# Optimization experiments

Hardware: AMD Instinct MI355X
Metric: run time of the kernel (lower is better)

The kernel has to match this reference:

```python
import jax, jax.numpy as jnp
import numpy as np

N, L, D = 2, 2048, 1024
H, KV, HD = 16, 4, 64
CAP = 50.0


def _rope_cache(L, hd):
    inv_freq = 1.0 / (10000.0 ** (np.arange(0, hd, 2, dtype=np.float32) / hd))
    t = np.arange(L, dtype=np.float32)
    freqs = np.outer(t, inv_freq)                      # (L, hd/2)
    emb = np.concatenate([freqs, freqs], axis=-1)      # (L, hd)
    return jnp.asarray(np.cos(emb)), jnp.asarray(np.sin(emb))


def setup_inputs() -> dict:
    key = jax.random.key(0)
    ks = jax.random.split(key, 6)
    s = 0.02
    cos, sin = _rope_cache(L, HD)
    return {
        "x": jax.random.normal(ks[0], (N, L, D), jnp.float32),
        "Wq": jax.random.normal(ks[1], (D, H * HD), jnp.float32) * s,
        "bq": jnp.zeros((H * HD,), jnp.float32),
        "Wk": jax.random.normal(ks[2], (D, KV * HD), jnp.float32) * s,
        "bk": jnp.zeros((KV * HD,), jnp.float32),
        "Wv": jax.random.normal(ks[3], (D, KV * HD), jnp.float32) * s,
        "bv": jnp.zeros((KV * HD,), jnp.float32),
        "Wo": jax.random.normal(ks[4], (D, D), jnp.float32) * s,
        "bo": jnp.zeros((D,), jnp.float32),
        "q_gamma": jnp.ones((H, HD), jnp.float32),
        "k_gamma": jnp.ones((KV, HD), jnp.float32),
        "rope_cos": cos,
        "rope_sin": sin,
        "is_causal": 1,
    }


def _rmsnorm(t, gamma):
    # t: (N, heads, L, HD); gamma: (heads, HD)
    inv = jax.lax.rsqrt(jnp.mean(t * t, axis=-1, keepdims=True) + 1e-6)
    return t * inv * gamma[None, :, None, :]


def _apply_rope(t, cos, sin):
    # t: (N, heads, L, HD); cos/sin: (L, HD)
    hd = t.shape[-1]
    t1, t2 = t[..., : hd // 2], t[..., hd // 2:]
    rot = jnp.concatenate([-t2, t1], axis=-1)
    return t * cos[None, None] + rot * sin[None, None]


def reference(x, Wq, bq, Wk, bk, Wv, bv, Wo, bo, q_gamma, k_gamma, rope_cos, rope_sin, is_causal):
    n, l, d = x.shape
    h, hd = q_gamma.shape
    kv = k_gamma.shape[0]
    n_rep = h // kv

    q = (x @ Wq + bq).reshape(n, l, h, hd).transpose(0, 2, 1, 3)   # (n,h,l,hd)
    k = (x @ Wk + bk).reshape(n, l, kv, hd).transpose(0, 2, 1, 3)  # (n,kv,l,hd)
    v = (x @ Wv + bv).reshape(n, l, kv, hd).transpose(0, 2, 1, 3)

    q = _rmsnorm(q, q_gamma)
    k = _rmsnorm(k, k_gamma)
    q = _apply_rope(q, rope_cos, rope_sin)
    k = _apply_rope(k, rope_cos, rope_sin)

    if n_rep > 1:
        k = jnp.repeat(k, n_rep, axis=1)
        v = jnp.repeat(v, n_rep, axis=1)

    scale = hd ** -0.5
    logits = jnp.einsum("bhqd,bhkd->bhqk", q, k) * scale
    logits = CAP * jnp.tanh(logits / CAP)
    if is_causal:
        causal = jnp.tril(jnp.ones((l, l), dtype=bool))
        logits = jnp.where(causal[None, None], logits, -jnp.inf)
    weights = jax.nn.softmax(logits, axis=-1)
    y = jnp.einsum("bhqk,bhkd->bhqd", weights, v)
    y = y.transpose(0, 2, 1, 3).reshape(n, l, d)
    return y @ Wo + bo
```

## Files before the change

kernel.cpp:

```cpp
#include <hip/hip_runtime.h>
#include <hip/hip_bf16.h>

typedef __attribute__((ext_vector_type(8))) short short8;
typedef __attribute__((ext_vector_type(4))) float f32x4;

using bf16 = __hip_bfloat16;

#define L_SEQ 2048
#define NB 2
#define DM 1024
#define NH 16
#define NKV 4
#define HDIM 64
#define CAPV 50.0f

#if __has_builtin(__builtin_amdgcn_exp2f)
#define EXP2(x) __builtin_amdgcn_exp2f(x)
#else
#define EXP2(x) exp2f(x)
#endif

__device__ __forceinline__ unsigned short f2bs(float f) {
  bf16 h = __float2bfloat16(f);
  return __builtin_bit_cast(unsigned short, h);
}

__device__ __forceinline__ float bs2f(unsigned short u) {
  return __bfloat162float(__builtin_bit_cast(bf16, u));
}

__device__ __forceinline__ void gload_lds16(const void* g, void* l) {
  __builtin_amdgcn_global_load_lds(
      (const __attribute__((address_space(1))) void*)g,
      (__attribute__((address_space(3))) void*)l, 16, 0, 0);
}

__global__ void k_cvt_x(const float* __restrict__ x, ushort* __restrict__ xb) {
  int i = (blockIdx.x * blockDim.x + threadIdx.x) * 4;
  float4 v = *reinterpret_cast<const float4*>(x + i);
  ushort4 o = make_ushort4(f2bs(v.x), f2bs(v.y), f2bs(v.z), f2bs(v.w));
  *reinterpret_cast<ushort4*>(xb + i) = o;
}

__global__ void k_transpose_all(const float* __restrict__ Wq, const float* __restrict__ Wk,
                                const float* __restrict__ Wv, const float* __restrict__ Wo,
                                bf16* __restrict__ wqt, bf16* __restrict__ wkt,
                                bf16* __restrict__ wvt, bf16* __restrict__ wot) {
  __shared__ float tile[32][33];
  const int z = blockIdx.z;
  const float* W = (z == 0) ? Wq : (z == 1) ? Wk : (z == 2) ? Wv : Wo;
  bf16* Wt = (z == 0) ? wqt : (z == 1) ? wkt : (z == 2) ? wvt : wot;
  const int Ncols = (z == 1 || z == 2) ? 256 : 1024;
  const int bx = blockIdx.x * 32;
  if (bx >= Ncols) return;
  const int by = blockIdx.y * 32;
  const int tx = threadIdx.x, ty = threadIdx.y;
  #pragma unroll
  for (int j = 0; j < 32; j += 8)
    tile[ty + j][tx] = W[(size_t)(by + ty + j) * Ncols + bx + tx];
  __syncthreads();
  #pragma unroll
  for (int j = 0; j < 32; j += 8)
    Wt[(size_t)(bx + ty + j) * 1024 + by + tx] = __float2bfloat16(tile[tx][ty + j]);
}

template<int OUT_MODE>
__global__ __launch_bounds__(256) void k_gemm(const bf16* __restrict__ A,
                                              const bf16* __restrict__ Bt,
                                              const float* __restrict__ bq,
                                              const float* __restrict__ bk,
                                              const float* __restrict__ bv,
                                              const float* __restrict__ qg,
                                              const float* __restrict__ kg,
                                              const float* __restrict__ rcT,
                                              const float* __restrict__ rsT,
                                              void* __restrict__ out0,
                                              void* __restrict__ out1,
                                              void* __restrict__ out2,
                                              int M, int Ncols, int K) {
  __shared__ __align__(16) bf16 As[2][64 * 64];
  __shared__ __align__(16) bf16 Bs[2][128 * 64];
  const int t = threadIdx.x;
  const int lane = t & 63;
  const int w = t >> 6;
  const int wr = w >> 1, wc = w & 1;
  const int m0 = blockIdx.y * 64, n0 = blockIdx.x * 128;
  const int lr = lane & 15, lg = lane >> 4;
  const int nkt = K >> 6;

  f32x4 acc[2][4];
  #pragma unroll
  for (int m = 0; m < 2; ++m)
    #pragma unroll
    for (int n = 0; n < 4; ++n)
      acc[m][n] = f32x4{0.f, 0.f, 0.f, 0.f};

  {
    #pragma unroll
    for (int p = 0; p < 2; ++p) {
      const int Gb = p * 256 + w * 64;
      const int G = Gb + lane;
      const int row = G >> 3, gc = G & 7;
      gload_lds16(&A[(size_t)(m0 + row) * K + ((gc ^ (row & 7)) * 8)], &As[0][Gb * 8]);
    }
    #pragma unroll
    for (int p = 0; p < 4; ++p) {
      const int Gb = p * 256 + w * 64;
      const int G = Gb + lane;
      const int row = G >> 3, gc = G & 7;
      gload_lds16(&Bt[(size_t)(n0 + row) * K + ((gc ^ (row & 7)) * 8)], &Bs[0][Gb * 8]);
    }
  }
  int cur = 0;

  for (int kt = 0; kt < nkt; ++kt) {
    __syncthreads();

    if (kt + 1 < nkt) {
      const int kofs = (kt + 1) * 64;
      #pragma unroll
      for (int p = 0; p < 2; ++p) {
        const int Gb = p * 256 + w * 64;
        const int G = Gb + lane;
        const int row = G >> 3, gc = G & 7;
        gload_lds16(&A[(size_t)(m0 + row) * K + kofs + ((gc ^ (row & 7)) * 8)],
                    &As[cur ^ 1][Gb * 8]);
      }
      #pragma unroll
      for (int p = 0; p < 4; ++p) {
        const int Gb = p * 256 + w * 64;
        const int G = Gb + lane;
        const int row = G >> 3, gc = G & 7;
        gload_lds16(&Bt[(size_t)(n0 + row) * K + kofs + ((gc ^ (row & 7)) * 8)],
                    &Bs[cur ^ 1][Gb * 8]);
      }
    }

    #pragma unroll
    for (int ks = 0; ks < 2; ++ks) {
      short8 af[2], bfr[4];
      #pragma unroll
      for (int m = 0; m < 2; ++m) {
        const int row = wr * 32 + m * 16 + lr;
        af[m] = *reinterpret_cast<const short8*>(
            &As[cur][row * 64 + (((ks * 4 + lg) ^ (row & 7)) * 8)]);
      }
      #pragma unroll
      for (int n = 0; n < 4; ++n) {
        const int row = wc * 64 + n * 16 + lr;
        bfr[n] = *reinterpret_cast<const short8*>(
            &Bs[cur][row * 64 + (((ks * 4 + lg) ^ (row & 7)) * 8)]);
      }
      #pragma unroll
      for (int m = 0; m < 2; ++m)
        #pragma unroll
        for (int n = 0; n < 4; ++n)
          acc[m][n] = __builtin_amdgcn_mfma_f32_16x16x32_bf16(af[m], bfr[n], acc[m][n], 0, 0, 0);
    }
    cur ^= 1;
  }

  const int colbase = n0 + wc * 64;

  if (OUT_MODE == 1) {
    #pragma unroll
    for (int m = 0; m < 2; ++m) {
      const int row = m0 + wr * 32 + m * 16 + lg * 4;
      #pragma unroll
      for (int n = 0; n < 4; ++n) {
        const int col = colbase + n * 16 + lr;
        const float bvv = bq[col];
        #pragma unroll
        for (int r = 0; r < 4; ++r)
          reinterpret_cast<float*>(out0)[(size_t)(row + r) * Ncols + col] = acc[m][n][r] + bvv;
      }
    }
  } else {
    if (colbase >= 1280) {
      #pragma unroll
      for (int m = 0; m < 2; ++m) {
        const int row = m0 + wr * 32 + m * 16 + lg * 4;
        const int bb = row >> 11, l = row & 2047;
        #pragma unroll
        for (int n = 0; n < 4; ++n) {
          const int d = colbase - 1280 + n * 16 + lr;
          const float bvv = bv[d];
          ushort4 o;
          o.x = f2bs(acc[m][n][0] + bvv);
          o.y = f2bs(acc[m][n][1] + bvv);
          o.z = f2bs(acc[m][n][2] + bvv);
          o.w = f2bs(acc[m][n][3] + bvv);
          *reinterpret_cast<ushort4*>(
              &reinterpret_cast<bf16*>(out2)[((size_t)bb * 256 + d) * L_SEQ + l]) = o;
        }
      }
    } else {
      const bool isQ = (colbase < 1024);
      const float* bias = isQ ? bq : bk;
      const float* gma = isQ ? qg : kg;
      bf16* dst0 = reinterpret_cast<bf16*>(isQ ? out0 : out1);
      const int cb = isQ ? colbase : (colbase - 1024);
      const int head = cb >> 6;
      const int heads = isQ ? NH : NKV;
      float g[4];
      #pragma unroll
      for (int n = 0; n < 4; ++n) g[n] = gma[cb + n * 16 + lr];
      #pragma unroll
      for (int m = 0; m < 2; ++m) {
        const int row = m0 + wr * 32 + m * 16 + lg * 4;
        float vv[4][4];
        float ss[4] = {0.f, 0.f, 0.f, 0.f};
        #pragma unroll
        for (int n = 0; n < 4; ++n) {
          const float bvv = bias[cb + n * 16 + lr];
          #pragma unroll
          for (int r = 0; r < 4; ++r) {
            vv[n][r] = acc[m][n][r] + bvv;
            ss[r] = fmaf(vv[n][r], vv[n][r], ss[r]);
          }
        }
        #pragma unroll
        for (int r = 0; r < 4; ++r) {
          float s = ss[r];
          s += __shfl_xor(s, 1, 64);
          s += __shfl_xor(s, 2, 64);
          s += __shfl_xor(s, 4, 64);
          s += __shfl_xor(s, 8, 64);
          ss[r] = rsqrtf(s * (1.0f / 64.0f) + 1e-6f);
        }
        float tv[4][4];
        #pragma unroll
        for (int n = 0; n < 4; ++n)
          #pragma unroll
          for (int r = 0; r < 4; ++r)
            tv[n][r] = vv[n][r] * ss[r] * g[n];
        #pragma unroll
        for (int r = 0; r < 4; ++r) {
          const int grow = row + r;
          const int bb = grow >> 11, l = grow & 2047;
          bf16* dst = dst0 + (((size_t)bb * heads + head) * L_SEQ + l) * HDIM;
          #pragma unroll
          for (int n = 0; n < 4; ++n) {
            const int d = n * 16 + lr;
            const float c = rcT[l * HDIM + d];
            const float s2 = rsT[l * HDIM + d];
            const float rot = (n < 2) ? -tv[n ^ 2][r] : tv[n ^ 2][r];
            dst[d] = __float2bfloat16(fmaf(tv[n][r], c, rot * s2));
          }
        }
      }
    }
  }
}

__global__ __launch_bounds__(256) void k_attn(
    const bf16* __restrict__ qb, const bf16* __restrict__ kb,
    const bf16* __restrict__ vt, bf16* __restrict__ y,
    bf16* __restrict__ pO, float* __restrict__ pd,
    const int* __restrict__ causal_flag) {
  __shared__ __align__(16) bf16 Ks[2][64 * 64];
  __shared__ __align__(16) bf16 Vs[2][64 * 64];
  __shared__ __align__(16) bf16 Ps[4 * 16 * 64];

  const int t = threadIdx.x, lane = t & 63, w = t >> 6;
  const int lr = lane & 15, lg = lane >> 4;
  const int jx = blockIdx.x;
  const int bh = blockIdx.y;
  const int half = blockIdx.z;
  const int b = bh >> 4, h = bh & 15;
  const int kvh = h >> 2;
  const bool causal = (*causal_flag) != 0;

  const int T_a = causal ? (2 * jx + 2) : 32;
  const int T_b = causal ? (32 - 2 * jx) : 32;
  const int total = T_a + T_b;
  const int mid = (total + 1) >> 1;
  const int g0 = half ? mid : 0;
  const int g1 = half ? total : mid;

  const bf16* kbase = kb + ((size_t)b * NKV + kvh) * L_SEQ * HDIM;
  const bf16* vbase = vt + ((size_t)b * NKV + kvh) * HDIM * L_SEQ;

  for (int seg = 0; seg < 2; ++seg) {
    const int qp = seg ? (15 - jx) : jx;
    const int ts = seg ? T_b : T_a;
    const int base = seg ? T_a : 0;
    const int lo = max(0, g0 - base);
    const int hi = min(ts, g1 - base);
    if (lo >= hi) continue;

    const int q0 = qp * 128;
    const int wrow = q0 + w * 32;

    short8 qf[2][2];
    #pragma unroll
    for (int s = 0; s < 2; ++s) {
      const bf16* qrow = qb + (((size_t)bh) * L_SEQ + wrow + s * 16 + lr) * HDIM;
      qf[s][0] = *reinterpret_cast<const short8*>(qrow + lg * 8);
      qf[s][1] = *reinterpret_cast<const short8*>(qrow + 32 + lg * 8);
    }

    f32x4 o0[4], o1[4];
    #pragma unroll
    for (int n = 0; n < 4; ++n) {
      o0[n] = f32x4{0.f, 0.f, 0.f, 0.f};
      o1[n] = f32x4{0.f, 0.f, 0.f, 0.f};
    }
    float plt0 = 0.f, plt1 = 0.f;

    __syncthreads();
    {
      const int k00 = lo * 64;
      #pragma unroll
      for (int i = 0; i < 2; ++i) {
        const int Gb = i * 256 + w * 64;
        const int G = Gb + lane;
        const int row = G >> 3, gc = G & 7;
        gload_lds16(kbase + (size_t)(k00 + row) * HDIM + ((gc ^ (row & 7)) * 8), &Ks[0][Gb * 8]);
        gload_lds16(vbase + (size_t)row * L_SEQ + k00 + ((gc ^ (row & 7)) * 8), &Vs[0][Gb * 8]);
      }
    }
    int cur = 0;

    for (int kt = lo; kt < hi; ++kt) {
      __syncthreads();

      if (kt + 1 < hi) {
        const int k0n = (kt + 1) * 64;
        #pragma unroll
        for (int i = 0; i < 2; ++i) {
          const int Gb = i * 256 + w * 64;
          const int G = Gb + lane;
          const int row = G >> 3, gc = G & 7;
          gload_lds16(kbase + (size_t)(k0n + row) * HDIM + ((gc ^ (row & 7)) * 8),
                      &Ks[cur ^ 1][Gb * 8]);
          gload_lds16(vbase + (size_t)row * L_SEQ + k0n + ((gc ^ (row & 7)) * 8),
                      &Vs[cur ^ 1][Gb * 8]);
        }
      }

      f32x4 s0[4], s1[4];
      #pragma unroll
      for (int n = 0; n < 4; ++n) {
        s0[n] = f32x4{0.f, 0.f, 0.f, 0.f};
        s1[n] = f32x4{0.f, 0.f, 0.f, 0.f};
      }
      #pragma unroll
      for (int n = 0; n < 4; ++n) {
        const int krow = n * 16 + lr;
        short8 kf0 = *reinterpret_cast<const short8*>(
            &Ks[cur][krow * 64 + ((lg ^ (krow & 7)) * 8)]);
        short8 kf1 = *reinterpret_cast<const short8*>(
            &Ks[cur][krow * 64 + (((4 + lg) ^ (krow & 7)) * 8)]);
        s0[n] = __builtin_amdgcn_mfma_f32_16x16x32_bf16(kf0, qf[0][0], s0[n], 0, 0, 0);
        s0[n] = __builtin_amdgcn_mfma_f32_16x16x32_bf16(kf1, qf[0][1], s0[n], 0, 0, 0);
        s1[n] = __builtin_amdgcn_mfma_f32_16x16x32_bf16(kf0, qf[1][0], s1[n], 0, 0, 0);
        s1[n] = __builtin_amdgcn_mfma_f32_16x16x32_bf16(kf1, qf[1][1], s1[n], 0, 0, 0);
      }

      const int k0 = kt * 64;
      #pragma unroll
      for (int n = 0; n < 4; ++n) {
        #pragma unroll
        for (int r = 0; r < 4; ++r) {
          float xs = s0[n][r];
          s0[n][r] = fmaf(xs * 0.18033688f, fmaf(xs * xs, -2.0833333e-6f, 1.0f), -16.0f);
          xs = s1[n][r];
          s1[n][r] = fmaf(xs * 0.18033688f, fmaf(xs * xs, -2.0833333e-6f, 1.0f), -16.0f);
        }
      }
      if (causal && (k0 + 63 > wrow)) {
        #pragma unroll
        for (int n = 0; n < 4; ++n) {
          const int keyb = k0 + n * 16 + lg * 4;
          #pragma unroll
          for (int r = 0; r < 4; ++r)
            if (keyb + r > wrow + lr) s0[n][r] = -1e30f;
        }
      }
      if (causal && (k0 + 63 > wrow + 16)) {
        #pragma unroll
        for (int n = 0; n < 4; ++n) {
          const int keyb = k0 + n * 16 + lg * 4;
          #pragma unroll
          for (int r = 0; r < 4; ++r)
            if (keyb + r > wrow + 16 + lr) s1[n][r] = -1e30f;
        }
      }

      short8 pf0[2], pf1[2];
      #pragma unroll
      for (int n = 0; n < 4; ++n) {
        const float p0 = EXP2(s0[n][0]);
        const float p1 = EXP2(s0[n][1]);
        const float p2 = EXP2(s0[n][2]);
        const float p3 = EXP2(s0[n][3]);
        plt0 += (p0 + p1) + (p2 + p3);
        ushort4 pk = make_ushort4(f2bs(p0), f2bs(p1), f2bs(p2), f2bs(p3));
        *reinterpret_cast<ushort4*>(
            &Ps[w * 1024 + lr * 64 + (((4 * n + lg) ^ (lr & 14)) * 4)]) = pk;
      }
      pf0[0] = *reinterpret_cast<const short8*>(
          &Ps[w * 1024 + lr * 64 + (((2 * lg) ^ (lr & 14)) * 4)]);
      pf0[1] = *reinterpret_cast<const short8*>(
          &Ps[w * 1024 + lr * 64 + (((8 + 2 * lg) ^ (lr & 14)) * 4)]);
      #pragma unroll
      for (int n = 0; n < 4; ++n) {
        const float p0 = EXP2(s1[n][0]);
        const float p1 = EXP2(s1[n][1]);
        const float p2 = EXP2(s1[n][2]);
        const float p3 = EXP2(s1[n][3]);
        plt1 += (p0 + p1) + (p2 + p3);
        ushort4 pk = make_ushort4(f2bs(p0), f2bs(p1), f2bs(p2), f2bs(p3));
        *reinterpret_cast<ushort4*>(
            &Ps[w * 1024 + lr * 64 + (((4 * n + lg) ^ (lr & 14)) * 4)]) = pk;
      }
      pf1[0] = *reinterpret_cast<const short8*>(
          &Ps[w * 1024 + lr * 64 + (((2 * lg) ^ (lr & 14)) * 4)]);
      pf1[1] = *reinterpret_cast<const short8*>(
          &Ps[w * 1024 + lr * 64 + (((8 + 2 * lg) ^ (lr & 14)) * 4)]);

      #pragma unroll
      for (int ks = 0; ks < 2; ++ks) {
        #pragma unroll
        for (int n = 0; n < 4; ++n) {
          const int vd = n * 16 + lr;
          short8 vfr = *reinterpret_cast<const short8*>(
              &Vs[cur][vd * 64 + (((ks * 4 + lg) ^ (vd & 7)) * 8)]);
          o0[n] = __builtin_amdgcn_mfma_f32_16x16x32_bf16(pf0[ks], vfr, o0[n], 0, 0, 0);
          o1[n] = __builtin_amdgcn_mfma_f32_16x16x32_bf16(pf1[ks], vfr, o1[n], 0, 0, 0);
        }
      }
      cur ^= 1;
    }

    const bool full = (lo == 0) && (hi == ts);
    #pragma unroll
    for (int s = 0; s < 2; ++s) {
      float ls = s ? plt1 : plt0;
      ls += __shfl_xor(ls, 16, 64);
      ls += __shfl_xor(ls, 32, 64);
      const f32x4* oa = s ? o1 : o0;
      if (full) {
        #pragma unroll
        for (int r = 0; r < 4; ++r) {
          const float den = __shfl(ls, lg * 4 + r, 64);
          const float invl = __builtin_amdgcn_rcpf(den);
          const int qg_ = wrow + s * 16 + lg * 4 + r;
          #pragma unroll
          for (int n = 0; n < 4; ++n)
            y[((size_t)b * L_SEQ + qg_) * DM + h * HDIM + n * 16 + lr] =
                __float2bfloat16(oa[n][r] * invl);
        }
      } else {
        if (lane < 16)
          pd[((size_t)half * NB * NH + bh) * L_SEQ + wrow + s * 16 + lane] = ls;
        #pragma unroll
        for (int r = 0; r < 4; ++r) {
          const int qg_ = wrow + s * 16 + lg * 4 + r;
          #pragma unroll
          for (int n = 0; n < 4; ++n)
            pO[(((size_t)half * NB + b) * L_SEQ + qg_) * DM + h * HDIM + n * 16 + lr] =
                __float2bfloat16(oa[n][r]);
        }
      }
    }
  }
}

__global__ __launch_bounds__(256) void k_combine(const bf16* __restrict__ pO,
                                                 const float* __restrict__ pd,
                                                 bf16* __restrict__ y,
                                                 const int* __restrict__ causal_flag) {
  if ((*causal_flag) == 0) return;
  const int b = blockIdx.x >> 10;
  const int l = 1024 + (blockIdx.x & 1023);
  const int c4 = threadIdx.x * 4;
  const int h = c4 >> 6;
  const float d0 = pd[((size_t)b * NH + h) * L_SEQ + l];
  const float d1 = pd[((size_t)NB * NH + b * NH + h) * L_SEQ + l];
  const float inv = __builtin_amdgcn_rcpf(d0 + d1);
  const size_t base0 = ((size_t)b * L_SEQ + l) * DM + c4;
  const size_t base1 = (((size_t)NB + b) * L_SEQ + l) * DM + c4;
  ushort4 a = *reinterpret_cast<const ushort4*>(reinterpret_cast<const ushort*>(pO) + base0);
  ushort4 bb = *reinterpret_cast<const ushort4*>(reinterpret_cast<const ushort*>(pO) + base1);
  ushort4 o;
  o.x = f2bs((bs2f(a.x) + bs2f(bb.x)) * inv);
  o.y = f2bs((bs2f(a.y) + bs2f(bb.y)) * inv);
  o.z = f2bs((bs2f(a.z) + bs2f(bb.z)) * inv);
  o.w = f2bs((bs2f(a.w) + bs2f(bb.w)) * inv);
  *reinterpret_cast<ushort4*>(reinterpret_cast<ushort*>(y) +
                              ((size_t)b * L_SEQ + l) * DM + c4) = o;
}

extern "C" void kernel_launch(void* const* d_in, const int* in_sizes, int n_in,
                              void* d_out, int out_size, void* d_ws, size_t ws_size,
                              hipStream_t stream) {
  (void)in_sizes; (void)n_in; (void)out_size; (void)ws_size;
  const float* x  = (const float*)d_in[0];
  const float* Wq = (const float*)d_in[1];
  const float* bq = (const float*)d_in[2];
  const float* Wk = (const float*)d_in[3];
  const float* bk = (const float*)d_in[4];
  const float* Wv = (const float*)d_in[5];
  const float* bv = (const float*)d_in[6];
  const float* Wo = (const float*)d_in[7];
  const float* bo = (const float*)d_in[8];
  const float* qg = (const float*)d_in[9];
  const float* kg = (const float*)d_in[10];
  const float* rc = (const float*)d_in[11];
  const float* rs = (const float*)d_in[12];
  const int* causal = (const int*)d_in[13];
  float* out = (float*)d_out;

  char* ws = (char*)d_ws;
  size_t off = 0;
  auto alloc = [&](size_t bytes) -> char* {
    char* p = ws + off;
    off += (bytes + 255) & ~(size_t)255;
    return p;
  };
  bf16* xb    = (bf16*)alloc((size_t)4096 * 1024 * 2);
  bf16* wqkvt = (bf16*)alloc((size_t)1536 * 1024 * 2);
  bf16* wot   = (bf16*)alloc((size_t)1024 * 1024 * 2);
  bf16* vt    = (bf16*)alloc((size_t)NB * NKV * HDIM * L_SEQ * 2);
  bf16* qb    = (bf16*)alloc((size_t)NB * NH * L_SEQ * HDIM * 2);
  bf16* kb    = (bf16*)alloc((size_t)NB * NKV * L_SEQ * HDIM * 2);
  bf16* y     = (bf16*)alloc((size_t)4096 * 1024 * 2);
  bf16* pO    = (bf16*)alloc((size_t)2 * NB * L_SEQ * DM * 2);
  float* pd   = (float*)alloc((size_t)2 * NB * NH * L_SEQ * 4);
  bf16* wqt   = wqkvt;
  bf16* wkt   = wqkvt + (size_t)1024 * 1024;
  bf16* wvt   = wqkvt + (size_t)1280 * 1024;

  k_cvt_x<<<4096, 256, 0, stream>>>(x, (ushort*)xb);
  k_transpose_all<<<dim3(32, 32, 4), dim3(32, 8), 0, stream>>>(Wq, Wk, Wv, Wo, wqt, wkt, wvt, wot);

  k_gemm<6><<<dim3(12, 64), 256, 0, stream>>>(xb, wqkvt, bq, bk, bv, qg, kg, rc, rs,
                                              qb, kb, vt, 4096, 1536, 1024);

  k_attn<<<dim3(8, NB * NH, 2), 256, 0, stream>>>(qb, kb, vt, y, pO, pd, causal);
  k_combine<<<NB * 1024, 256, 0, stream>>>(pO, pd, y, causal);

  k_gemm<1><<<dim3(8, 64), 256, 0, stream>>>(y, wot, bo, nullptr, nullptr, nullptr, nullptr,
                                             nullptr, nullptr, out, nullptr, nullptr,
                                             4096, 1024, 1024);
}
```

Baseline: 98.57 us.

## Keep softmax probabilities in registers and permute V reads to match MFMA layout

Removes the LDS round trip for the P tile: probabilities are packed to bf16 with v_cvt_pk_bf16_f32 and fed directly as MFMA A operands. To make the register layout of P line up with the k-dimension of the PV product, the V fragment is now assembled from two 8-byte LDS reads at permuted offsets. This drops LDS writes and reads per tile and frees the Ps shared buffer, at the cost of twice as many (narrower) V LDS loads.

After: 96.06 us. 1.03x faster.

```diff
diff --git a/kernel.cpp b/kernel.cpp
--- a/kernel.cpp
+++ b/kernel.cpp
@@ -3,6 +3,7 @@
 
 typedef __attribute__((ext_vector_type(8))) short short8;
 typedef __attribute__((ext_vector_type(4))) float f32x4;
+typedef __attribute__((ext_vector_type(4))) unsigned int u32x4;
 
 using bf16 = __hip_bfloat16;
 
@@ -27,6 +28,12 @@
 
 __device__ __forceinline__ float bs2f(unsigned short u) {
   return __bfloat162float(__builtin_bit_cast(bf16, u));
+}
+
+__device__ __forceinline__ unsigned int cvt_pk_bf16(float lo, float hi) {
+  unsigned int w;
+  asm("v_cvt_pk_bf16_f32 %0, %1, %2" : "=v"(w) : "v"(lo), "v"(hi));
+  return w;
 }
 
 __device__ __forceinline__ void gload_lds16(const void* g, void* l) {
@@ -260,7 +267,6 @@
     const int* __restrict__ causal_flag) {
   __shared__ __align__(16) bf16 Ks[2][64 * 64];
   __shared__ __align__(16) bf16 Vs[2][64 * 64];
-  __shared__ __align__(16) bf16 Ps[4 * 16 * 64];
 
   const int t = threadIdx.x, lane = t & 63, w = t >> 6;
   const int lr = lane & 15, lg = lane >> 4;
@@ -388,45 +394,48 @@
         }
       }
 
+      unsigned int w0[8], w1[8];
+      #pragma unroll
+      for (int n = 0; n < 4; ++n) {
+        const float a0 = EXP2(s0[n][0]);
+        const float a1 = EXP2(s0[n][1]);
+        const float a2 = EXP2(s0[n][2]);
+        const float a3 = EXP2(s0[n][3]);
+        plt0 += (a0 + a1) + (a2 + a3);
+        w0[2 * n] = cvt_pk_bf16(a0, a1);
+        w0[2 * n + 1] = cvt_pk_bf16(a2, a3);
+        const float c0 = EXP2(s1[n][0]);
+        const float c1 = EXP2(s1[n][1]);
+        const float c2 = EXP2(s1[n][2]);
+        const float c3 = EXP2(s1[n][3]);
+        plt1 += (c0 + c1) + (c2 + c3);
+        w1[2 * n] = cvt_pk_bf16(c0, c1);
+        w1[2 * n + 1] = cvt_pk_bf16(c2, c3);
+      }
       short8 pf0[2], pf1[2];
       #pragma unroll
-      for (int n = 0; n < 4; ++n) {
-        const float p0 = EXP2(s0[n][0]);
-        const float p1 = EXP2(s0[n][1]);
-        const float p2 = EXP2(s0[n][2]);
-        const float p3 = EXP2(s0[n][3]);
-        plt0 += (p0 + p1) + (p2 + p3);
-        ushort4 pk = make_ushort4(f2bs(p0), f2bs(p1), f2bs(p2), f2bs(p3));
-        *reinterpret_cast<ushort4*>(
-            &Ps[w * 1024 + lr * 64 + (((4 * n + lg) ^ (lr & 14)) * 4)]) = pk;
-      }
-      pf0[0] = *reinterpret_cast<const short8*>(
-          &Ps[w * 1024 + lr * 64 + (((2 * lg) ^ (lr & 14)) * 4)]);
-      pf0[1] = *reinterpret_cast<const short8*>(
-          &Ps[w * 1024 + lr * 64 + (((8 + 2 * lg) ^ (lr & 14)) * 4)]);
-      #pragma unroll
-      for (int n = 0; n < 4; ++n) {
-        const float p0 = EXP2(s1[n][0]);
-        const float p1 = EXP2(s1[n][1]);
-        const float p2 = EXP2(s1[n][2]);
-        const float p3 = EXP2(s1[n][3]);
-        plt1 += (p0 + p1) + (p2 + p3);
-        ushort4 pk = make_ushort4(f2bs(p0), f2bs(p1), f2bs(p2), f2bs(p3));
-        *reinterpret_cast<ushort4*>(
-            &Ps[w * 1024 + lr * 64 + (((4 * n + lg) ^ (lr & 14)) * 4)]) = pk;
-      }
-      pf1[0] = *reinterpret_cast<const short8*>(
-          &Ps[w * 1024 + lr * 64 + (((2 * lg) ^ (lr & 14)) * 4)]);
-      pf1[1] = *reinterpret_cast<const short8*>(
-          &Ps[w * 1024 + lr * 64 + (((8 + 2 * lg) ^ (lr & 14)) * 4)]);
-
-      #pragma unroll
       for (int ks = 0; ks < 2; ++ks) {
+        u32x4 a = {w0[4 * ks], w0[4 * ks + 1], w0[4 * ks + 2], w0[4 * ks + 3]};
+        u32x4 c = {w1[4 * ks], w1[4 * ks + 1], w1[4 * ks + 2], w1[4 * ks + 3]};
+        pf0[ks] = __builtin_bit_cast(short8, a);
+        pf1[ks] = __builtin_bit_cast(short8, c);
+      }
+
+      const int voff = 4 * (lg & 1);
+      #pragma unroll
+      for (int ks = 0; ks < 2; ++ks) {
+        const int gA = 4 * ks + (lg >> 1);
         #pragma unroll
         for (int n = 0; n < 4; ++n) {
           const int vd = n * 16 + lr;
-          short8 vfr = *reinterpret_cast<const short8*>(
-              &Vs[cur][vd * 64 + (((ks * 4 + lg) ^ (vd & 7)) * 8)]);
+          const int vb_ = vd * 64;
+          const int sw = vd & 7;
+          const uint2 vlo = *reinterpret_cast<const uint2*>(
+              &Vs[cur][vb_ + ((gA ^ sw) * 8 + voff)]);
+          const uint2 vhi = *reinterpret_cast<const uint2*>(
+              &Vs[cur][vb_ + (((gA + 2) ^ sw) * 8 + voff)]);
+          u32x4 vv = {vlo.x, vlo.y, vhi.x, vhi.y};
+          short8 vfr = __builtin_bit_cast(short8, vv);
           o0[n] = __builtin_amdgcn_mfma_f32_16x16x32_bf16(pf0[ks], vfr, o0[n], 0, 0, 0);
           o1[n] = __builtin_amdgcn_mfma_f32_16x16x32_bf16(pf1[ks], vfr, o1[n], 0, 0, 0);
         }
```
